# Performance work log

Measured on AMD Instinct MI355X. Metric: run time of the kernel, lower is better.

Reference implementation:

```python
import jax, jax.numpy as jnp
import numpy as np


def setup_inputs() -> dict:
    key = jax.random.key(0)
    ks = jax.random.split(key, 10)
    B, T, E = 4096, 200, 64
    H0, H1, H2 = 80, 40, 1
    D = 4 * E  # concat feature dim = 256
    glorot = lambda k, shp: jax.random.normal(k, shp, jnp.float32) * jnp.sqrt(2.0 / (shp[0] + shp[1]))
    return {
        "queries": jax.random.normal(ks[0], (B, 1, E), jnp.float32),
        "keys": jax.random.normal(ks[1], (B, T, E), jnp.float32),
        "keys_length": jax.random.randint(ks[2], (B, 1), 0, T, jnp.int32),
        "W0": glorot(ks[3], (D, H0)),
        "b0": jnp.zeros((H0,), jnp.float32),
        "W1": glorot(ks[4], (H0, H1)),
        "b1": jnp.zeros((H1,), jnp.float32),
        "W2": glorot(ks[5], (H1, H2)),
        "b2": jnp.zeros((H2,), jnp.float32),
    }


def reference(queries, keys, keys_length, W0, b0, W1, b1, W2, b2):
    B, T, E = keys.shape
    # repeat query along history axis: [B,1,E] -> [B,T,E]
    q = jnp.broadcast_to(queries, (B, T, E))
    # DIN attention input: [B,T,4E]
    att = jnp.concatenate([q, keys, q - keys, q * keys], axis=-1)
    # tiny 3-layer MLP, sigmoid activations (att_activation, no output_activation override)
    h = jax.nn.sigmoid(att @ W0 + b0)
    h = jax.nn.sigmoid(h @ W1 + b1)
    score = jax.nn.sigmoid(h @ W2 + b2)          # [B,T,1]
    out = jnp.transpose(score, (0, 2, 1))         # [B,1,T]
    # sequence mask: [B,1,T]
    key_masks = jnp.arange(T)[None, None, :] < keys_length[:, :, None]
    # weight_normalization=False -> masked positions become 0, no softmax
    out = jnp.where(key_masks, out, jnp.zeros_like(out))
    # weighted sum over history: [B,1,T] @ [B,T,E] -> [B,1,E]
    return jnp.matmul(out, keys)
```

## Files before the change

kernel.cpp:

```cpp
#include <hip/hip_runtime.h>
#include <hip/hip_bf16.h>

#define NT 256

typedef __attribute__((ext_vector_type(8))) short short8;
typedef __attribute__((ext_vector_type(4))) float f32x4;

__device__ __forceinline__ float b2f(unsigned short u) {
  return __uint_as_float(((unsigned int)u) << 16);
}
__device__ __forceinline__ unsigned short f2b(float f) {
  unsigned int x = __float_as_uint(f);
  return (unsigned short)((x + 0x7fffu + ((x >> 16) & 1u)) >> 16);
}
__device__ __forceinline__ float sigmoidf(float x) {
  return __builtin_amdgcn_rcpf(1.0f + __expf(-x));
}

__global__ __launch_bounds__(NT, 2) void prep_c(
    const float* __restrict__ q, const float* __restrict__ W0,
    const float* __restrict__ b0, float* __restrict__ C, int B)
{
  __shared__ float Wac[64 * 80];
  __shared__ float qlds[32 * 64];
  const int bbase = blockIdx.x * 32, tid = threadIdx.x;
  for (int idx = tid; idx < 5120; idx += NT) {
    const int e = idx / 80, h = idx - e * 80;
    Wac[idx] = W0[e * 80 + h] + W0[(128 + e) * 80 + h];
  }
  for (int idx = tid; idx < 2048; idx += NT) {
    const int bl = idx >> 6, e = idx & 63;
    const int bg = bbase + bl;
    qlds[idx] = (bg < B) ? q[bg * 64 + e] : 0.0f;
  }
  __syncthreads();
  #pragma unroll
  for (int i = 0; i < 10; ++i) {
    const int idx = tid + i * NT;
    const int bl = idx / 80, h = idx - bl * 80;
    const int bg = bbase + bl;
    if (bg < B) {
      float acc = b0[h];
      #pragma unroll 8
      for (int e = 0; e < 64; ++e) acc += qlds[bl * 64 + e] * Wac[e * 80 + h];
      C[bg * 80 + h] = acc;
    }
  }
}

#define PK 72
#define PW 72
#define PH 104
#define PW1 104
__global__ __launch_bounds__(NT, 3) void din_attn_main(
    const float* __restrict__ q,
    const float* __restrict__ keys,
    const int* __restrict__ klen,
    const float* __restrict__ W0,
    const float* __restrict__ b0,
    const float* __restrict__ W1,
    const float* __restrict__ b1,
    const float* __restrict__ W2,
    const float* __restrict__ b2,
    float* __restrict__ out,
    const float* __restrict__ Cpre)
{
  const int b = blockIdx.x;
  const int tid = threadIdx.x;

  __shared__ __align__(16) unsigned short kbuf[64 * PK];
  __shared__ __align__(16) unsigned short WbT[80 * PW];
  __shared__ __align__(16) unsigned short h0[64 * PH];
  __shared__ __align__(16) unsigned short W1T[48 * PW1];
  __shared__ __align__(16) float cf[80];
  __shared__ __align__(16) float b1f[48];
  __shared__ __align__(16) float w2f[48];
  __shared__ __align__(16) float qf[64];
  __shared__ __align__(16) float score[64];
  __shared__ __align__(16) float part[256];
  __shared__ float b2v;

  int L = klen[b];
  L = max(0, min(200, L));

  if (tid < 64) qf[tid] = q[b * 64 + tid];
  if (tid == 0) b2v = b2[0];
  __syncthreads();

  for (int idx = tid; idx < 5120; idx += NT) {
    const int e = idx / 80, h = idx - e * 80;
    const float v = W0[(64 + e) * 80 + h] - W0[(128 + e) * 80 + h]
                    + qf[e] * W0[(192 + e) * 80 + h];
    WbT[h * PW + e] = f2b(v);
  }
  if (Cpre != nullptr) {
    if (tid < 80) cf[tid] = Cpre[b * 80 + tid];
  } else if (tid < 80) {
    float acc = b0[tid];
    #pragma unroll 8
    for (int e = 0; e < 64; ++e)
      acc += qf[e] * (W0[e * 80 + tid] + W0[(128 + e) * 80 + tid]);
    cf[tid] = acc;
  }
  for (int idx = tid; idx < 48 * PW1; idx += NT) {
    const int j = idx / PW1, h = idx - j * PW1;
    W1T[idx] = (j < 40 && h < 80) ? f2b(W1[h * 40 + j]) : (unsigned short)0;
  }
  for (int idx = tid; idx < (64 * PK) / 2; idx += NT) ((unsigned int*)kbuf)[idx] = 0u;
  for (int idx = tid; idx < (64 * PH) / 2; idx += NT) ((unsigned int*)h0)[idx] = 0u;
  if (tid < 48) {
    b1f[tid] = (tid < 40) ? b1[tid] : 0.0f;
    w2f[tid] = (tid < 40) ? W2[tid] : 0.0f;
  }
  __syncthreads();

  const int lane = tid & 63;
  const int wv = tid >> 6;
  const int lm = lane & 15;
  const int quad = lane >> 4;
  const int m = wv * 16 + lm;
  const int e_ep = tid & 63;
  const int stripe = tid >> 6;
  float wacc = 0.0f;
  const int passes = (L + 63) >> 6;

  for (int p = 0; p < passes; ++p) {
    const int nr = min(64, L - (p << 6));
    {
      const float4* src = (const float4*)(keys + (size_t)b * 12800 + ((size_t)p << 12));
      const int nch = nr * 16;
      for (int idx = tid; idx < nch; idx += NT) {
        const int row = idx >> 4, c = idx & 15;
        float4 v = src[row * 16 + c];
        ushort4 o;
        o.x = f2b(v.x); o.y = f2b(v.y); o.z = f2b(v.z); o.w = f2b(v.w);
        *(ushort4*)&kbuf[row * PK + c * 4] = o;
      }
    }
    __syncthreads();

    {
      const short8 a0 = *(const short8*)&kbuf[m * PK + quad * 8];
      const short8 a1 = *(const short8*)&kbuf[m * PK + 32 + quad * 8];
      #pragma unroll
      for (int nt = 0; nt < 5; ++nt) {
        const int col = nt * 16 + lm;
        const float cv = cf[col];
        f32x4 acc;
        acc[0] = cv; acc[1] = cv; acc[2] = cv; acc[3] = cv;
        const short8 w0f = *(const short8*)&WbT[col * PW + quad * 8];
        const short8 w1f = *(const short8*)&WbT[col * PW + 32 + quad * 8];
        acc = __builtin_amdgcn_mfma_f32_16x16x32_bf16(a0, w0f, acc, 0, 0, 0);
        acc = __builtin_amdgcn_mfma_f32_16x16x32_bf16(a1, w1f, acc, 0, 0, 0);
        #pragma unroll
        for (int r = 0; r < 4; ++r)
          h0[(wv * 16 + quad * 4 + r) * PH + col] = f2b(sigmoidf(acc[r]));
      }
    }
    __syncthreads();

    {
      const short8 ha0 = *(const short8*)&h0[m * PH + quad * 8];
      const short8 ha1 = *(const short8*)&h0[m * PH + 32 + quad * 8];
      const short8 ha2 = *(const short8*)&h0[m * PH + 64 + quad * 8];
      float pd[4] = {0.0f, 0.0f, 0.0f, 0.0f};
      #pragma unroll
      for (int nt = 0; nt < 3; ++nt) {
        const int col = nt * 16 + lm;
        const float bv = b1f[col];
        f32x4 acc;
        acc[0] = bv; acc[1] = bv; acc[2] = bv; acc[3] = bv;
        const short8 wb0 = *(const short8*)&W1T[col * PW1 + quad * 8];
        const short8 wb1 = *(const short8*)&W1T[col * PW1 + 32 + quad * 8];
        const short8 wb2 = *(const short8*)&W1T[col * PW1 + 64 + quad * 8];
        acc = __builtin_amdgcn_mfma_f32_16x16x32_bf16(ha0, wb0, acc, 0, 0, 0);
        acc = __builtin_amdgcn_mfma_f32_16x16x32_bf16(ha1, wb1, acc, 0, 0, 0);
        acc = __builtin_amdgcn_mfma_f32_16x16x32_bf16(ha2, wb2, acc, 0, 0, 0);
        const float wj = w2f[col];
        #pragma unroll
        for (int r = 0; r < 4; ++r) pd[r] += sigmoidf(acc[r]) * wj;
      }
      #pragma unroll
      for (int r = 0; r < 4; ++r) {
        pd[r] += __shfl_xor(pd[r], 1);
        pd[r] += __shfl_xor(pd[r], 2);
        pd[r] += __shfl_xor(pd[r], 4);
        pd[r] += __shfl_xor(pd[r], 8);
      }
      if (lm == 0) {
        #pragma unroll
        for (int r = 0; r < 4; ++r)
          score[wv * 16 + quad * 4 + r] = sigmoidf(pd[r] + b2v);
      }
    }
    __syncthreads();

    #pragma unroll
    for (int i = 0; i < 16; ++i) {
      const int t = stripe + 4 * i;
      if (t < nr) wacc += score[t] * b2f(kbuf[t * PK + e_ep]);
    }
    __syncthreads();
  }

  part[tid] = wacc;
  __syncthreads();
  if (tid < 64) {
    out[b * 64 + tid] =
        part[tid] + part[64 + tid] + part[128 + tid] + part[192 + tid];
  }
}

extern "C" void kernel_launch(void* const* d_in, const int* in_sizes, int n_in,
                              void* d_out, int out_size, void* d_ws, size_t ws_size,
                              hipStream_t stream) {
  const int B = in_sizes[2];
  const float* Cpre = nullptr;
  if (ws_size >= (size_t)B * 80 * sizeof(float)) {
    float* C = (float*)d_ws;
    prep_c<<<(B + 31) / 32, NT, 0, stream>>>(
        (const float*)d_in[0], (const float*)d_in[3], (const float*)d_in[4], C, B);
    Cpre = C;
  }
  din_attn_main<<<B, NT, 0, stream>>>(
      (const float*)d_in[0], (const float*)d_in[1], (const int*)d_in[2],
      (const float*)d_in[3], (const float*)d_in[4], (const float*)d_in[5],
      (const float*)d_in[6], (const float*)d_in[7], (const float*)d_in[8],
      (float*)d_out, Cpre);
}
```

Baseline: 376.3 us.

## Assign one wave per batch row with register-resident key tiles and no block syncs

After: 514.5 us. 36.7% more time.

```diff
diff --git a/kernel.cpp b/kernel.cpp
--- a/kernel.cpp
+++ b/kernel.cpp
@@ -1,14 +1,14 @@
 #include <hip/hip_runtime.h>
-#include <hip/hip_bf16.h>
-
-#define NT 256
+
+#define NT 512
+#define NWAVE 8
+#define PE 136
+#define PW1 104
+#define PH 104
 
 typedef __attribute__((ext_vector_type(8))) short short8;
 typedef __attribute__((ext_vector_type(4))) float f32x4;
 
-__device__ __forceinline__ float b2f(unsigned short u) {
-  return __uint_as_float(((unsigned int)u) << 16);
-}
 __device__ __forceinline__ unsigned short f2b(float f) {
   unsigned int x = __float_as_uint(f);
   return (unsigned short)((x + 0x7fffu + ((x >> 16) & 1u)) >> 16);
@@ -16,19 +16,33 @@
 __device__ __forceinline__ float sigmoidf(float x) {
   return __builtin_amdgcn_rcpf(1.0f + __expf(-x));
 }
-
-__global__ __launch_bounds__(NT, 2) void prep_c(
+__device__ __forceinline__ short8 pack8(float4 a, float4 b) {
+  short8 r;
+  r[0] = (short)f2b(a.x); r[1] = (short)f2b(a.y); r[2] = (short)f2b(a.z); r[3] = (short)f2b(a.w);
+  r[4] = (short)f2b(b.x); r[5] = (short)f2b(b.y); r[6] = (short)f2b(b.z); r[7] = (short)f2b(b.w);
+  return r;
+}
+__device__ __forceinline__ short8 pack8q(float4 a, float4 b, float4 qa, float4 qb) {
+  short8 r;
+  r[0] = (short)f2b(a.x * qa.x); r[1] = (short)f2b(a.y * qa.y);
+  r[2] = (short)f2b(a.z * qa.z); r[3] = (short)f2b(a.w * qa.w);
+  r[4] = (short)f2b(b.x * qb.x); r[5] = (short)f2b(b.y * qb.y);
+  r[6] = (short)f2b(b.z * qb.z); r[7] = (short)f2b(b.w * qb.w);
+  return r;
+}
+
+__global__ __launch_bounds__(256, 2) void prep_c(
     const float* __restrict__ q, const float* __restrict__ W0,
     const float* __restrict__ b0, float* __restrict__ C, int B)
 {
   __shared__ float Wac[64 * 80];
   __shared__ float qlds[32 * 64];
   const int bbase = blockIdx.x * 32, tid = threadIdx.x;
-  for (int idx = tid; idx < 5120; idx += NT) {
+  for (int idx = tid; idx < 5120; idx += 256) {
     const int e = idx / 80, h = idx - e * 80;
     Wac[idx] = W0[e * 80 + h] + W0[(128 + e) * 80 + h];
   }
-  for (int idx = tid; idx < 2048; idx += NT) {
+  for (int idx = tid; idx < 2048; idx += 256) {
     const int bl = idx >> 6, e = idx & 63;
     const int bg = bbase + bl;
     qlds[idx] = (bg < B) ? q[bg * 64 + e] : 0.0f;
@@ -36,7 +50,7 @@
   __syncthreads();
   #pragma unroll
   for (int i = 0; i < 10; ++i) {
-    const int idx = tid + i * NT;
+    const int idx = tid + i * 256;
     const int bl = idx / 80, h = idx - bl * 80;
     const int bg = bbase + bl;
     if (bg < B) {
@@ -48,11 +62,7 @@
   }
 }
 
-#define PK 72
-#define PW 72
-#define PH 104
-#define PW1 104
-__global__ __launch_bounds__(NT, 3) void din_attn_main(
+__global__ __launch_bounds__(NT, 4) void din_attn_main(
     const float* __restrict__ q,
     const float* __restrict__ keys,
     const int* __restrict__ klen,
@@ -63,152 +73,163 @@
     const float* __restrict__ W2,
     const float* __restrict__ b2,
     float* __restrict__ out,
-    const float* __restrict__ Cpre)
+    const float* __restrict__ Cpre,
+    int B)
 {
-  const int b = blockIdx.x;
+  __shared__ __align__(16) unsigned short WxT[80 * PE];
+  __shared__ __align__(16) unsigned short W1T[48 * PW1];
+  __shared__ __align__(16) unsigned short h0s[NWAVE][16 * PH];
+
   const int tid = threadIdx.x;
 
-  __shared__ __align__(16) unsigned short kbuf[64 * PK];
-  __shared__ __align__(16) unsigned short WbT[80 * PW];
-  __shared__ __align__(16) unsigned short h0[64 * PH];
-  __shared__ __align__(16) unsigned short W1T[48 * PW1];
-  __shared__ __align__(16) float cf[80];
-  __shared__ __align__(16) float b1f[48];
-  __shared__ __align__(16) float w2f[48];
-  __shared__ __align__(16) float qf[64];
-  __shared__ __align__(16) float score[64];
-  __shared__ __align__(16) float part[256];
-  __shared__ float b2v;
-
-  int L = klen[b];
-  L = max(0, min(200, L));
-
-  if (tid < 64) qf[tid] = q[b * 64 + tid];
-  if (tid == 0) b2v = b2[0];
-  __syncthreads();
-
-  for (int idx = tid; idx < 5120; idx += NT) {
+  for (int idx = tid; idx < 128 * 80; idx += NT) {
     const int e = idx / 80, h = idx - e * 80;
-    const float v = W0[(64 + e) * 80 + h] - W0[(128 + e) * 80 + h]
-                    + qf[e] * W0[(192 + e) * 80 + h];
-    WbT[h * PW + e] = f2b(v);
-  }
-  if (Cpre != nullptr) {
-    if (tid < 80) cf[tid] = Cpre[b * 80 + tid];
-  } else if (tid < 80) {
-    float acc = b0[tid];
-    #pragma unroll 8
-    for (int e = 0; e < 64; ++e)
-      acc += qf[e] * (W0[e * 80 + tid] + W0[(128 + e) * 80 + tid]);
-    cf[tid] = acc;
+    const float v = (e < 64)
+        ? (W0[(64 + e) * 80 + h] - W0[(128 + e) * 80 + h])
+        : W0[(128 + e) * 80 + h];
+    WxT[h * PE + e] = f2b(v);
   }
   for (int idx = tid; idx < 48 * PW1; idx += NT) {
     const int j = idx / PW1, h = idx - j * PW1;
     W1T[idx] = (j < 40 && h < 80) ? f2b(W1[h * 40 + j]) : (unsigned short)0;
   }
-  for (int idx = tid; idx < (64 * PK) / 2; idx += NT) ((unsigned int*)kbuf)[idx] = 0u;
-  for (int idx = tid; idx < (64 * PH) / 2; idx += NT) ((unsigned int*)h0)[idx] = 0u;
-  if (tid < 48) {
-    b1f[tid] = (tid < 40) ? b1[tid] : 0.0f;
-    w2f[tid] = (tid < 40) ? W2[tid] : 0.0f;
+  {
+    const int w0i = tid >> 6, ln = tid & 63;
+    for (int i = ln; i < 256; i += 64)
+      h0s[w0i][(i >> 4) * PH + 80 + (i & 15)] = 0;
   }
   __syncthreads();
 
+  const int wv = __builtin_amdgcn_readfirstlane(tid >> 6);
   const int lane = tid & 63;
-  const int wv = tid >> 6;
   const int lm = lane & 15;
   const int quad = lane >> 4;
-  const int m = wv * 16 + lm;
-  const int e_ep = tid & 63;
-  const int stripe = tid >> 6;
-  float wacc = 0.0f;
-  const int passes = (L + 63) >> 6;
-
-  for (int p = 0; p < passes; ++p) {
-    const int nr = min(64, L - (p << 6));
-    {
-      const float4* src = (const float4*)(keys + (size_t)b * 12800 + ((size_t)p << 12));
-      const int nch = nr * 16;
-      for (int idx = tid; idx < nch; idx += NT) {
-        const int row = idx >> 4, c = idx & 15;
-        float4 v = src[row * 16 + c];
-        ushort4 o;
-        o.x = f2b(v.x); o.y = f2b(v.y); o.z = f2b(v.z); o.w = f2b(v.w);
-        *(ushort4*)&kbuf[row * PK + c * 4] = o;
-      }
-    }
-    __syncthreads();
-
-    {
-      const short8 a0 = *(const short8*)&kbuf[m * PK + quad * 8];
-      const short8 a1 = *(const short8*)&kbuf[m * PK + 32 + quad * 8];
+  const int b = blockIdx.x * NWAVE + wv;
+  if (b >= B) return;
+
+  int L = klen[b];
+  L = __builtin_amdgcn_readfirstlane(max(0, min(200, L)));
+  unsigned short* h0 = h0s[wv];
+
+  const float* qb = q + (size_t)b * 64;
+  const float4* q4 = (const float4*)qb;
+  const float4 q0 = q4[quad * 2],     q1 = q4[quad * 2 + 1];
+  const float4 q2 = q4[8 + quad * 2], q3 = q4[8 + quad * 2 + 1];
+
+  float cfv[5];
+  if (Cpre != nullptr) {
+    #pragma unroll
+    for (int nt = 0; nt < 5; ++nt) cfv[nt] = Cpre[b * 80 + nt * 16 + lm];
+  } else {
+    #pragma unroll
+    for (int nt = 0; nt < 5; ++nt) cfv[nt] = b0[nt * 16 + lm];
+    for (int e = 0; e < 64; ++e) {
+      const float qv = qb[e];
       #pragma unroll
       for (int nt = 0; nt < 5; ++nt) {
         const int col = nt * 16 + lm;
-        const float cv = cf[col];
-        f32x4 acc;
-        acc[0] = cv; acc[1] = cv; acc[2] = cv; acc[3] = cv;
-        const short8 w0f = *(const short8*)&WbT[col * PW + quad * 8];
-        const short8 w1f = *(const short8*)&WbT[col * PW + 32 + quad * 8];
-        acc = __builtin_amdgcn_mfma_f32_16x16x32_bf16(a0, w0f, acc, 0, 0, 0);
-        acc = __builtin_amdgcn_mfma_f32_16x16x32_bf16(a1, w1f, acc, 0, 0, 0);
-        #pragma unroll
-        for (int r = 0; r < 4; ++r)
-          h0[(wv * 16 + quad * 4 + r) * PH + col] = f2b(sigmoidf(acc[r]));
+        cfv[nt] += qv * (W0[e * 80 + col] + W0[(128 + e) * 80 + col]);
       }
     }
-    __syncthreads();
-
-    {
-      const short8 ha0 = *(const short8*)&h0[m * PH + quad * 8];
-      const short8 ha1 = *(const short8*)&h0[m * PH + 32 + quad * 8];
-      const short8 ha2 = *(const short8*)&h0[m * PH + 64 + quad * 8];
-      float pd[4] = {0.0f, 0.0f, 0.0f, 0.0f};
+  }
+  float b1v[3], w2v[3];
+  #pragma unroll
+  for (int nt = 0; nt < 3; ++nt) {
+    const int col = nt * 16 + lm;
+    b1v[nt] = (col < 40) ? b1[col] : 0.0f;
+    w2v[nt] = (col < 40) ? W2[col] : 0.0f;
+  }
+  const float b2v = b2[0];
+
+  const float* kb = keys + (size_t)b * 12800;
+  float wacc = 0.0f;
+  const int ntile = (L + 15) >> 4;
+
+  const float4 z4 = {0.0f, 0.0f, 0.0f, 0.0f};
+  float4 k0 = z4, k1 = z4, k2 = z4, k3 = z4;
+  if (ntile > 0 && lm < L) {
+    const float4* kp = (const float4*)(kb + (size_t)lm * 64);
+    k0 = kp[quad * 2]; k1 = kp[quad * 2 + 1];
+    k2 = kp[8 + quad * 2]; k3 = kp[8 + quad * 2 + 1];
+  }
+
+  for (int p = 0; p < ntile; ++p) {
+    const short8 a0  = pack8(k0, k1);
+    const short8 a1  = pack8(k2, k3);
+    const short8 aq0 = pack8q(k0, k1, q0, q1);
+    const short8 aq1 = pack8q(k2, k3, q2, q3);
+
+    if (p + 1 < ntile) {
+      const int t = ((p + 1) << 4) + lm;
+      if (t < L) {
+        const float4* kp = (const float4*)(kb + (size_t)t * 64);
+        k0 = kp[quad * 2]; k1 = kp[quad * 2 + 1];
+        k2 = kp[8 + quad * 2]; k3 = kp[8 + quad * 2 + 1];
+      } else { k0 = k1 = k2 = k3 = z4; }
+    }
+
+    #pragma unroll
+    for (int nt = 0; nt < 5; ++nt) {
+      const int col = nt * 16 + lm;
+      const unsigned short* wr = &WxT[col * PE + quad * 8];
+      const short8 w0 = *(const short8*)(wr);
+      const short8 w1 = *(const short8*)(wr + 32);
+      const short8 w2 = *(const short8*)(wr + 64);
+      const short8 w3 = *(const short8*)(wr + 96);
+      f32x4 acc;
+      acc[0] = cfv[nt]; acc[1] = cfv[nt]; acc[2] = cfv[nt]; acc[3] = cfv[nt];
+      acc = __builtin_amdgcn_mfma_f32_16x16x32_bf16(a0,  w0, acc, 0, 0, 0);
+      acc = __builtin_amdgcn_mfma_f32_16x16x32_bf16(a1,  w1, acc, 0, 0, 0);
+      acc = __builtin_amdgcn_mfma_f32_16x16x32_bf16(aq0, w2, acc, 0, 0, 0);
+      acc = __builtin_amdgcn_mfma_f32_16x16x32_bf16(aq1, w3, acc, 0, 0, 0);
       #pragma unroll
-      for (int nt = 0; nt < 3; ++nt) {
-        const int col = nt * 16 + lm;
-        const float bv = b1f[col];
-        f32x4 acc;
-        acc[0] = bv; acc[1] = bv; acc[2] = bv; acc[3] = bv;
-        const short8 wb0 = *(const short8*)&W1T[col * PW1 + quad * 8];
-        const short8 wb1 = *(const short8*)&W1T[col * PW1 + 32 + quad * 8];
-        const short8 wb2 = *(const short8*)&W1T[col * PW1 + 64 + quad * 8];
-        acc = __builtin_amdgcn_mfma_f32_16x16x32_bf16(ha0, wb0, acc, 0, 0, 0);
-        acc = __builtin_amdgcn_mfma_f32_16x16x32_bf16(ha1, wb1, acc, 0, 0, 0);
-        acc = __builtin_amdgcn_mfma_f32_16x16x32_bf16(ha2, wb2, acc, 0, 0, 0);
-        const float wj = w2f[col];
-        #pragma unroll
-        for (int r = 0; r < 4; ++r) pd[r] += sigmoidf(acc[r]) * wj;
+      for (int r = 0; r < 4; ++r)
+        h0[(quad * 4 + r) * PH + col] = f2b(sigmoidf(acc[r]));
+    }
+
+    const short8 ha0 = *(const short8*)&h0[lm * PH + quad * 8];
+    const short8 ha1 = *(const short8*)&h0[lm * PH + 32 + quad * 8];
+    const short8 ha2 = *(const short8*)&h0[lm * PH + 64 + quad * 8];
+    float pd[4] = {0.0f, 0.0f, 0.0f, 0.0f};
+    #pragma unroll
+    for (int nt = 0; nt < 3; ++nt) {
+      const int col = nt * 16 + lm;
+      const unsigned short* wr = &W1T[col * PW1 + quad * 8];
+      const short8 wb0 = *(const short8*)(wr);
+      const short8 wb1 = *(const short8*)(wr + 32);
+      const short8 wb2 = *(const short8*)(wr + 64);
+      f32x4 acc;
+      acc[0] = b1v[nt]; acc[1] = b1v[nt]; acc[2] = b1v[nt]; acc[3] = b1v[nt];
+      acc = __builtin_amdgcn_mfma_f32_16x16x32_bf16(ha0, wb0, acc, 0, 0, 0);
+      acc = __builtin_amdgcn_mfma_f32_16x16x32_bf16(ha1, wb1, acc, 0, 0, 0);
+      acc = __builtin_amdgcn_mfma_f32_16x16x32_bf16(ha2, wb2, acc, 0, 0, 0);
+      #pragma unroll
+      for (int r = 0; r < 4; ++r) pd[r] += sigmoidf(acc[r]) * w2v[nt];
+    }
+    #pragma unroll
+    for (int r = 0; r < 4; ++r) {
+      pd[r] += __shfl_xor(pd[r], 1);
+      pd[r] += __shfl_xor(pd[r], 2);
+      pd[r] += __shfl_xor(pd[r], 4);
+      pd[r] += __shfl_xor(pd[r], 8);
+    }
+    float sc[4];
+    #pragma unroll
+    for (int r = 0; r < 4; ++r) sc[r] = sigmoidf(pd[r] + b2v);
+
+    const int t0 = p << 4;
+    const int nr = min(16, L - t0);
+    const float* krow = kb + (size_t)t0 * 64 + lane;
+    #pragma unroll
+    for (int t = 0; t < 16; ++t) {
+      if (t < nr) {
+        const float sv = __shfl(sc[t & 3], ((t >> 2) << 4) + lm);
+        wacc += sv * krow[(size_t)t * 64];
       }
-      #pragma unroll
-      for (int r = 0; r < 4; ++r) {
-        pd[r] += __shfl_xor(pd[r], 1);
-        pd[r] += __shfl_xor(pd[r], 2);
-        pd[r] += __shfl_xor(pd[r], 4);
-        pd[r] += __shfl_xor(pd[r], 8);
-      }
-      if (lm == 0) {
-        #pragma unroll
-        for (int r = 0; r < 4; ++r)
-          score[wv * 16 + quad * 4 + r] = sigmoidf(pd[r] + b2v);
-      }
-    }
-    __syncthreads();
-
-    #pragma unroll
-    for (int i = 0; i < 16; ++i) {
-      const int t = stripe + 4 * i;
-      if (t < nr) wacc += score[t] * b2f(kbuf[t * PK + e_ep]);
-    }
-    __syncthreads();
-  }
-
-  part[tid] = wacc;
-  __syncthreads();
-  if (tid < 64) {
-    out[b * 64 + tid] =
-        part[tid] + part[64 + tid] + part[128 + tid] + part[192 + tid];
-  }
+    }
+  }
+
+  out[(size_t)b * 64 + lane] = wacc;
 }
 
 extern "C" void kernel_launch(void* const* d_in, const int* in_sizes, int n_in,
@@ -218,13 +239,13 @@
   const float* Cpre = nullptr;
   if (ws_size >= (size_t)B * 80 * sizeof(float)) {
     float* C = (float*)d_ws;
-    prep_c<<<(B + 31) / 32, NT, 0, stream>>>(
+    prep_c<<<(B + 31) / 32, 256, 0, stream>>>(
         (const float*)d_in[0], (const float*)d_in[3], (const float*)d_in[4], C, B);
     Cpre = C;
   }
-  din_attn_main<<<B, NT, 0, stream>>>(
+  din_attn_main<<<(B + NWAVE - 1) / NWAVE, NT, 0, stream>>>(
       (const float*)d_in[0], (const float*)d_in[1], (const int*)d_in[2],
       (const float*)d_in[3], (const float*)d_in[4], (const float*)d_in[5],
       (const float*)d_in[6], (const float*)d_in[7], (const float*)d_in[8],
-      (float*)d_out, Cpre);
-}
+      (float*)d_out, Cpre, B);
+}
```
